# Performance work log

Hardware: AMD Instinct MI355X
Metric: run time of the kernel (lower is better)

Reference implementation:

```python
import jax, jax.numpy as jnp
import numpy as np

H = 128  # hidden_dim

def setup_inputs() -> dict:
    key = jax.random.key(0)
    ks = jax.random.split(key, 8)
    B, S = 32, 512
    return {
        "CNN_output": jax.random.normal(ks[0], (B, 4 * S, H), jnp.float32),
        "gaz_input": jax.random.normal(ks[1], (B, S, 128), jnp.float32),
        "gaz_input_back": jax.random.normal(ks[2], (B, S, 128), jnp.float32),
        "global_matrix": jax.random.normal(ks[3], (B, S, H), jnp.float32),
        "exper_input": jax.random.normal(ks[4], (B, S, H), jnp.float32),
        "W_cat": jax.random.normal(ks[5], (3 * H, 16 * H), jnp.float32) * (1.0 / np.sqrt(3 * H)),
        "b_cat": jnp.zeros((16 * H,), jnp.float32),
        "W_exp": jax.random.normal(ks[6], (H, 12 * H), jnp.float32) * (1.0 / np.sqrt(H)),
        "b_exp": jnp.zeros((12 * H,), jnp.float32),
    }


def _diag_gather(y, B, S, width):
    # y: [B, 4*S, 4*width]; for seq-block j pick columns j*width:(j+1)*width
    y = y.reshape(B, 4, S, 4, width)
    j = jnp.arange(4)
    y = y[:, j, :, j, :]              # [4, B, S, width]
    return jnp.transpose(y, (1, 0, 2, 3)).reshape(B, 4 * S, width)


def reference(CNN_output, gaz_input, gaz_input_back, global_matrix, exper_input,
              W_cat, b_cat, W_exp, b_exp):
    B, S4, _ = CNN_output.shape
    S = S4 // 4
    gaz = jnp.concatenate([gaz_input, gaz_input_back, gaz_input, gaz_input_back], axis=1)
    gm = jnp.tile(global_matrix, (1, 4, 1))
    exp_rep = jnp.tile(exper_input, (1, 4, 1))
    cat_in = jnp.concatenate([CNN_output, gaz, gm], axis=2)      # [B, 4S, 3H]
    cat_gates = _diag_gather(cat_in @ W_cat + b_cat, B, S, 4 * H)  # [B, 4S, 4H]
    exper_gates = _diag_gather(exp_rep @ W_exp + b_exp, B, S, 3 * H)  # [B, 4S, 3H]
    new_state = jnp.tanh(cat_gates[:, :, :H])
    gates = jax.nn.sigmoid(cat_gates[:, :, H:] + exper_gates)
    gates = jax.nn.softmax(gates.reshape(B, S4, 3, H), axis=2)
    state_cat = jnp.stack([new_state, CNN_output, exp_rep], axis=2)  # [B, 4S, 3, H]
    layer_output = jnp.sum(gates * state_cat, axis=2)                # [B, 4S, H]
    return tuple(layer_output[:, i * S:(i + 1) * S] for i in range(4))
```

## Files before the change

kernel.cpp:

```cpp
#include <hip/hip_runtime.h>

typedef unsigned short u16;
typedef unsigned int u32;
typedef short bf16x8 __attribute__((ext_vector_type(8)));
typedef float f32x4 __attribute__((ext_vector_type(4)));

#define HH 128

__device__ __forceinline__ u16 f2bf(float f) {
  u32 u = __float_as_uint(f);
  u += 0x7fffu + ((u >> 16) & 1u);
  return (u16)(u >> 16);
}
__device__ __forceinline__ u32 pack2(float a, float b) {
  return (u32)f2bf(a) | ((u32)f2bf(b) << 16);
}

__device__ __forceinline__ void lds_dma16(const void* g, void* l) {
  __builtin_amdgcn_global_load_lds(
      (const __attribute__((address_space(1))) u32*)g,
      (__attribute__((address_space(3))) u32*)l, 16, 0, 0);
}

__global__ __launch_bounds__(256) void prep_w(const float* __restrict__ Wcat,
                                              const float* __restrict__ Wexp,
                                              u16* __restrict__ Wc) {
  const int bx = blockIdx.x;
  const int nt = bx & 7;
  const int kc = (bx >> 3) & 15;
  const int q = bx >> 7;
  __shared__ u16 T[32 * 72];

  const int tid = threadIdx.x;
  const int r = tid >> 3;
  const int c8 = (tid & 7) * 8;
  float v[8];
  if (kc < 12) {
    const float* src =
        Wcat + (size_t)(kc * 32 + r) * 2048 + q * 512 + nt * 64 + c8;
    float4 a = *(const float4*)src;
    float4 b = *(const float4*)(src + 4);
    v[0] = a.x; v[1] = a.y; v[2] = a.z; v[3] = a.w;
    v[4] = b.x; v[5] = b.y; v[6] = b.z; v[7] = b.w;
  } else if (nt >= 2) {
    const float* src = Wexp + (size_t)((kc - 12) * 32 + r) * 1536 + q * 384 +
                       nt * 64 + c8 - 128;
    float4 a = *(const float4*)src;
    float4 b = *(const float4*)(src + 4);
    v[0] = a.x; v[1] = a.y; v[2] = a.z; v[3] = a.w;
    v[4] = b.x; v[5] = b.y; v[6] = b.z; v[7] = b.w;
  } else {
#pragma unroll
    for (int j = 0; j < 8; ++j) v[j] = 0.f;
  }
  uint4 pk;
  pk.x = pack2(v[0], v[1]);
  pk.y = pack2(v[2], v[3]);
  pk.z = pack2(v[4], v[5]);
  pk.w = pack2(v[6], v[7]);
  *(uint4*)&T[r * 72 + c8] = pk;
  __syncthreads();

  const int p = tid & 3;
  const int nl = tid >> 2;
  const int lq = p ^ (nl & 3) ^ ((nl >> 2) & 3);
  u16 w[8];
#pragma unroll
  for (int j = 0; j < 8; ++j) w[j] = T[(lq * 8 + j) * 72 + nl];
  uint4 o;
  o.x = (u32)w[0] | ((u32)w[1] << 16);
  o.y = (u32)w[2] | ((u32)w[3] << 16);
  o.z = (u32)w[4] | ((u32)w[5] << 16);
  o.w = (u32)w[6] | ((u32)w[7] << 16);
  const size_t idx = ((size_t)((q * 16 + kc) * 512) + nt * 64 + nl) * 4 + p;
  ((uint4*)Wc)[idx] = o;
}

__global__ __launch_bounds__(256, 3) void fused_gate(
    const float* __restrict__ CNN, const float* __restrict__ gaz,
    const float* __restrict__ gazb, const float* __restrict__ gm,
    const float* __restrict__ exper, const u16* __restrict__ Wc,
    const float* __restrict__ bcat, const float* __restrict__ bexp,
    float* __restrict__ out) {
  __shared__ u16 Abuf[64 * 32];
  __shared__ u16 Wbuf[256 * 32];

  const int tid = threadIdx.x;
  const int bx = blockIdx.x;
  const int half = bx & 1;
  const int tile = (bx >> 1) & 7;
  const int grp = bx >> 4;
  const int b = grp >> 2;
  const int q = grp & 3;
  const int s_base = tile * 64;
  const int h0 = half * 64;
  const int lane = tid & 63;
  const int wave = tid >> 6;
  const int l15 = lane & 15;
  const int quad = lane >> 4;
  const int physq = quad ^ (l15 & 3) ^ ((l15 >> 2) & 3);

  const int arow = tid >> 2;
  const int ap = tid & 3;
  const int alq = ap ^ (arow & 3) ^ ((arow >> 2) & 3);
  const int srow = s_base + arow;
  const float* s0 = CNN + (size_t)(b * 2048 + q * 512 + srow) * HH;
  const float* s1 = ((q & 1) ? gazb : gaz) + (size_t)(b * 512 + srow) * HH;
  const float* s2 = gm + (size_t)(b * 512 + srow) * HH;
  const float* s3 = exper + (size_t)(b * 512 + srow) * HH;

  const u16* wsrc = Wc + (size_t)q * 16 * 512 * 32;

  f32x4 acc[4][4];
#pragma unroll
  for (int rt = 0; rt < 4; ++rt)
#pragma unroll
    for (int gg = 0; gg < 4; ++gg) acc[rt][gg] = (f32x4)0.f;

  for (int kc = 0; kc < 16; ++kc) {
    const int k0 = kc * 32 + alq * 8;
    const int sel = k0 >> 7;
    const float* sp = (sel == 0) ? s0 : (sel == 1) ? s1 : (sel == 2) ? s2 : s3;
    sp += (k0 & 127);
    float4 f0 = *(const float4*)sp;
    float4 f1 = *(const float4*)(sp + 4);
    uint4 pk;
    pk.x = pack2(f0.x, f0.y);
    pk.y = pack2(f0.z, f0.w);
    pk.z = pack2(f1.x, f1.y);
    pk.w = pack2(f1.z, f1.w);
    *(uint4*)&Abuf[arow * 32 + ap * 8] = pk;

    const u16* wchunk = wsrc + (size_t)kc * 512 * 32;
#pragma unroll
    for (int i = 0; i < 4; ++i) {
      const int n0 = wave * 128 + h0 + i * 16;
      lds_dma16(wchunk + (size_t)n0 * 32 + lane * 8,
                &Wbuf[(wave * 64 + i * 16) * 32]);
    }
    __syncthreads();

    bf16x8 af[4];
#pragma unroll
    for (int rt = 0; rt < 4; ++rt)
      af[rt] = *(const bf16x8*)&Abuf[(rt * 16 + l15) * 32 + physq * 8];
    bf16x8 bfr[4];
#pragma unroll
    for (int gg = 0; gg < 4; ++gg) {
      const int c = gg * 64 + wave * 16 + l15;
      bfr[gg] = *(const bf16x8*)&Wbuf[c * 32 + physq * 8];
    }
#pragma unroll
    for (int rt = 0; rt < 4; ++rt)
#pragma unroll
      for (int gg = 0; gg < 4; ++gg)
        acc[rt][gg] = __builtin_amdgcn_mfma_f32_16x16x32_bf16(
            af[rt], bfr[gg], acc[rt][gg], 0, 0, 0);
    __syncthreads();
  }

  const float* bcq = bcat + q * 512;
  const float* beq = bexp + q * 384;
  const size_t cnnbase = (size_t)(b * 2048 + q * 512 + s_base) * HH;
  const size_t expbase = (size_t)(b * 512 + s_base) * HH;
  const size_t outbase = (size_t)((q * 32 + b) * 512 + s_base) * HH;
  const int h = h0 + wave * 16 + l15;
  const float bc0 = bcq[h];
  const float bc1 = bcq[128 + h];
  const float bc2 = bcq[256 + h];
  const float bc3 = bcq[384 + h];
  const float be1 = beq[h];
  const float be2 = beq[128 + h];
  const float be3 = beq[256 + h];
#pragma unroll
  for (int rt = 0; rt < 4; ++rt) {
#pragma unroll
    for (int r = 0; r < 4; ++r) {
      const int row = rt * 16 + quad * 4 + r;
      const float c0 = acc[rt][0][r] + bc0;
      const float p1 = acc[rt][1][r] + bc1 + be1;
      const float p2 = acc[rt][2][r] + bc2 + be2;
      const float p3 = acc[rt][3][r] + bc3 + be3;
      const float e2c = __expf(2.f * c0);
      const float ns = 1.f - 2.f * __builtin_amdgcn_rcpf(e2c + 1.f);
      const float g1 = __builtin_amdgcn_rcpf(1.f + __expf(-p1));
      const float g2 = __builtin_amdgcn_rcpf(1.f + __expf(-p2));
      const float g3 = __builtin_amdgcn_rcpf(1.f + __expf(-p3));
      const float e1 = __expf(g1);
      const float e2 = __expf(g2);
      const float e3 = __expf(g3);
      const float inv = __builtin_amdgcn_rcpf(e1 + e2 + e3);
      const float cnn = CNN[cnnbase + (size_t)row * HH + h];
      const float ex = exper[expbase + (size_t)row * HH + h];
      out[outbase + (size_t)row * HH + h] = (e1 * ns + e2 * cnn + e3 * ex) * inv;
    }
  }
}

extern "C" void kernel_launch(void* const* d_in, const int* in_sizes, int n_in,
                              void* d_out, int out_size, void* d_ws, size_t ws_size,
                              hipStream_t stream) {
  const float* CNN = (const float*)d_in[0];
  const float* gaz = (const float*)d_in[1];
  const float* gazb = (const float*)d_in[2];
  const float* gm = (const float*)d_in[3];
  const float* exper = (const float*)d_in[4];
  const float* Wcat = (const float*)d_in[5];
  const float* bcat = (const float*)d_in[6];
  const float* Wexp = (const float*)d_in[7];
  const float* bexp = (const float*)d_in[8];
  u16* Wc = (u16*)d_ws;

  prep_w<<<512, 256, 0, stream>>>(Wcat, Wexp, Wc);
  fused_gate<<<2048, 256, 0, stream>>>(CNN, gaz, gazb, gm, exper, Wc, bcat,
                                       bexp, (float*)d_out);
}
```

Before: 174.8 us.

## Preload full A tile into LDS, stream W from global with register prefetch

Loads the entire 64x512 activation tile into LDS once, with a swizzled layout, instead of per-k-chunk staging with two barriers per step. Weight fragments are read directly from global memory into registers and double-buffered across k steps, removing the LDS weight staging. The epilogue reuses the bf16 CNN and exper values from LDS instead of re-reading them in fp32 from global. This lowers precision of those terms and raises LDS use, which cuts occupancy to two blocks.

```diff
diff --git a/kernel.cpp b/kernel.cpp
--- a/kernel.cpp
+++ b/kernel.cpp
@@ -15,11 +15,8 @@
 __device__ __forceinline__ u32 pack2(float a, float b) {
   return (u32)f2bf(a) | ((u32)f2bf(b) << 16);
 }
-
-__device__ __forceinline__ void lds_dma16(const void* g, void* l) {
-  __builtin_amdgcn_global_load_lds(
-      (const __attribute__((address_space(1))) u32*)g,
-      (__attribute__((address_space(3))) u32*)l, 16, 0, 0);
+__device__ __forceinline__ float bf2f(u16 h) {
+  return __uint_as_float(((u32)h) << 16);
 }
 
 __global__ __launch_bounds__(256) void prep_w(const float* __restrict__ Wcat,
@@ -76,16 +73,17 @@
   ((uint4*)Wc)[idx] = o;
 }
 
-__global__ __launch_bounds__(256, 3) void fused_gate(
+__global__ __launch_bounds__(256, 2) void fused_gate(
     const float* __restrict__ CNN, const float* __restrict__ gaz,
     const float* __restrict__ gazb, const float* __restrict__ gm,
     const float* __restrict__ exper, const u16* __restrict__ Wc,
     const float* __restrict__ bcat, const float* __restrict__ bexp,
     float* __restrict__ out) {
-  __shared__ u16 Abuf[64 * 32];
-  __shared__ u16 Wbuf[256 * 32];
+  __shared__ u16 Abuf[16 * 64 * 32];
 
   const int tid = threadIdx.x;
+  const int lane = tid & 63;
+  const int wave = tid >> 6;
   const int bx = blockIdx.x;
   const int half = bx & 1;
   const int tile = (bx >> 1) & 7;
@@ -94,34 +92,18 @@
   const int q = grp & 3;
   const int s_base = tile * 64;
   const int h0 = half * 64;
-  const int lane = tid & 63;
-  const int wave = tid >> 6;
-  const int l15 = lane & 15;
-  const int quad = lane >> 4;
-  const int physq = quad ^ (l15 & 3) ^ ((l15 >> 2) & 3);
-
-  const int arow = tid >> 2;
-  const int ap = tid & 3;
-  const int alq = ap ^ (arow & 3) ^ ((arow >> 2) & 3);
-  const int srow = s_base + arow;
-  const float* s0 = CNN + (size_t)(b * 2048 + q * 512 + srow) * HH;
-  const float* s1 = ((q & 1) ? gazb : gaz) + (size_t)(b * 512 + srow) * HH;
-  const float* s2 = gm + (size_t)(b * 512 + srow) * HH;
-  const float* s3 = exper + (size_t)(b * 512 + srow) * HH;
-
-  const u16* wsrc = Wc + (size_t)q * 16 * 512 * 32;
-
-  f32x4 acc[4][4];
-#pragma unroll
-  for (int rt = 0; rt < 4; ++rt)
-#pragma unroll
-    for (int gg = 0; gg < 4; ++gg) acc[rt][gg] = (f32x4)0.f;
-
-  for (int kc = 0; kc < 16; ++kc) {
-    const int k0 = kc * 32 + alq * 8;
-    const int sel = k0 >> 7;
-    const float* sp = (sel == 0) ? s0 : (sel == 1) ? s1 : (sel == 2) ? s2 : s3;
-    sp += (k0 & 127);
+
+  const float* src_w =
+      (wave == 0) ? CNN + (size_t)(b * 2048 + q * 512 + s_base) * HH
+      : (wave == 1) ? (((q & 1) ? gazb : gaz) + (size_t)(b * 512 + s_base) * HH)
+      : (wave == 2) ? gm + (size_t)(b * 512 + s_base) * HH
+                    : exper + (size_t)(b * 512 + s_base) * HH;
+#pragma unroll
+  for (int t = 0; t < 16; ++t) {
+    const int s = t * 64 + lane;
+    const int row = s >> 4;
+    const int oct = s & 15;
+    const float* sp = src_w + (size_t)row * HH + oct * 8;
     float4 f0 = *(const float4*)sp;
     float4 f1 = *(const float4*)(sp + 4);
     uint4 pk;
@@ -129,40 +111,59 @@
     pk.y = pack2(f0.z, f0.w);
     pk.z = pack2(f1.x, f1.y);
     pk.w = pack2(f1.z, f1.w);
-    *(uint4*)&Abuf[arow * 32 + ap * 8] = pk;
-
-    const u16* wchunk = wsrc + (size_t)kc * 512 * 32;
-#pragma unroll
-    for (int i = 0; i < 4; ++i) {
-      const int n0 = wave * 128 + h0 + i * 16;
-      lds_dma16(wchunk + (size_t)n0 * 32 + lane * 8,
-                &Wbuf[(wave * 64 + i * 16) * 32]);
+    const int kc = wave * 4 + (oct >> 2);
+    const int o = oct & 3;
+    const int ph = o ^ ((row & 3) ^ ((row >> 2) & 3)) ^ wave;
+    *(uint4*)&Abuf[(kc * 64 + row) * 32 + ph * 8] = pk;
+  }
+  __syncthreads();
+
+  const int l15 = lane & 15;
+  const int quad = lane >> 4;
+  const int sl = (l15 & 3) ^ ((l15 >> 2) & 3);
+  const int physB = quad ^ sl;
+
+  const u16* wp[4];
+#pragma unroll
+  for (int gg = 0; gg < 4; ++gg) {
+    const int n = gg * 128 + h0 + wave * 16 + l15;
+    wp[gg] = Wc + (((size_t)(q * 16) * 512 + n) * 4 + physB) * 8;
+  }
+
+  f32x4 acc[4][4];
+#pragma unroll
+  for (int rt = 0; rt < 4; ++rt)
+#pragma unroll
+    for (int gg = 0; gg < 4; ++gg) acc[rt][gg] = (f32x4)0.f;
+
+  bf16x8 bcur[4], bnxt[4];
+#pragma unroll
+  for (int gg = 0; gg < 4; ++gg) bcur[gg] = *(const bf16x8*)wp[gg];
+
+#pragma unroll
+  for (int kc = 0; kc < 16; ++kc) {
+    if (kc < 15) {
+#pragma unroll
+      for (int gg = 0; gg < 4; ++gg)
+        bnxt[gg] = *(const bf16x8*)(wp[gg] + (size_t)(kc + 1) * 16384);
     }
-    __syncthreads();
-
+    const int pa = (quad ^ sl ^ (kc >> 2)) * 8;
     bf16x8 af[4];
 #pragma unroll
     for (int rt = 0; rt < 4; ++rt)
-      af[rt] = *(const bf16x8*)&Abuf[(rt * 16 + l15) * 32 + physq * 8];
-    bf16x8 bfr[4];
-#pragma unroll
-    for (int gg = 0; gg < 4; ++gg) {
-      const int c = gg * 64 + wave * 16 + l15;
-      bfr[gg] = *(const bf16x8*)&Wbuf[c * 32 + physq * 8];
-    }
+      af[rt] = *(const bf16x8*)&Abuf[(kc * 64 + rt * 16 + l15) * 32 + pa];
 #pragma unroll
     for (int rt = 0; rt < 4; ++rt)
 #pragma unroll
       for (int gg = 0; gg < 4; ++gg)
         acc[rt][gg] = __builtin_amdgcn_mfma_f32_16x16x32_bf16(
-            af[rt], bfr[gg], acc[rt][gg], 0, 0, 0);
-    __syncthreads();
+            af[rt], bcur[gg], acc[rt][gg], 0, 0, 0);
+#pragma unroll
+    for (int gg = 0; gg < 4; ++gg) bcur[gg] = bnxt[gg];
   }
 
   const float* bcq = bcat + q * 512;
   const float* beq = bexp + q * 384;
-  const size_t cnnbase = (size_t)(b * 2048 + q * 512 + s_base) * HH;
-  const size_t expbase = (size_t)(b * 512 + s_base) * HH;
   const size_t outbase = (size_t)((q * 32 + b) * 512 + s_base) * HH;
   const int h = h0 + wave * 16 + l15;
   const float bc0 = bcq[h];
@@ -172,11 +173,19 @@
   const float be1 = beq[h];
   const float be2 = beq[128 + h];
   const float be3 = beq[256 + h];
+  const int kcc = h >> 5;
+  const int kce = 12 + (h >> 5);
+  const int oh = (h >> 3) & 3;
+  const int he = h & 7;
 #pragma unroll
   for (int rt = 0; rt < 4; ++rt) {
 #pragma unroll
     for (int r = 0; r < 4; ++r) {
       const int row = rt * 16 + quad * 4 + r;
+      const int srw = (row & 3) ^ ((row >> 2) & 3);
+      const float cnn = bf2f(Abuf[(kcc * 64 + row) * 32 + (oh ^ srw) * 8 + he]);
+      const float ex =
+          bf2f(Abuf[(kce * 64 + row) * 32 + (oh ^ srw ^ 3) * 8 + he]);
       const float c0 = acc[rt][0][r] + bc0;
       const float p1 = acc[rt][1][r] + bc1 + be1;
       const float p2 = acc[rt][2][r] + bc2 + be2;
@@ -190,8 +199,6 @@
       const float e2 = __expf(g2);
       const float e3 = __expf(g3);
       const float inv = __builtin_amdgcn_rcpf(e1 + e2 + e3);
-      const float cnn = CNN[cnnbase + (size_t)row * HH + h];
-      const float ex = exper[expbase + (size_t)row * HH + h];
       out[outbase + (size_t)row * HH + h] = (e1 * ns + e2 * cnn + e3 * ex) * inv;
     }
   }
```

After: 169.9 us. 1.03x faster.
